# Kernel optimization log

Measured on AMD Instinct MI355X. Metric: run time of the kernel, lower is better.

Reference implementation:

```python
import jax, jax.numpy as jnp
from jax import lax
import numpy as np

GROUPS = 4


def _grid_sample_border(img, gx, gy):
    # img: [Bg, Cg, H, W]; gx, gy: [Bg, H, W] normalized grid in [-1, 1]
    # Replicates F.grid_sample(mode='bilinear', align_corners=False, padding_mode='border')
    Bg, Cg, H, W = img.shape
    ix = jnp.clip(((gx + 1.0) * W - 1.0) * 0.5, 0.0, W - 1.0)
    iy = jnp.clip(((gy + 1.0) * H - 1.0) * 0.5, 0.0, H - 1.0)
    x0 = jnp.floor(ix)
    y0 = jnp.floor(iy)
    wx = ix - x0
    wy = iy - y0
    x0i = x0.astype(jnp.int32)
    y0i = y0.astype(jnp.int32)
    x1i = jnp.minimum(x0i + 1, W - 1)
    y1i = jnp.minimum(y0i + 1, H - 1)

    def one(im, x0i, x1i, y0i, y1i, wx, wy):
        v00 = im[:, y0i, x0i]
        v01 = im[:, y0i, x1i]
        v10 = im[:, y1i, x0i]
        v11 = im[:, y1i, x1i]
        return (v00 * (1 - wx) * (1 - wy) + v01 * wx * (1 - wy)
                + v10 * (1 - wx) * wy + v11 * wx * wy)

    return jax.vmap(one)(img, x0i, x1i, y0i, y1i, wx, wy)


def setup_inputs() -> dict:
    key = jax.random.key(0)
    ks = jax.random.split(key, 8)
    B, N, C = 8, 4096, 768
    x = jax.random.normal(ks[0], (B, N, C), dtype=jnp.float32)
    dw_w = jax.random.normal(ks[1], (C, 1, 3, 3), dtype=jnp.float32) * 0.1  # depthwise kernel
    dw_b = jax.random.normal(ks[2], (C,), dtype=jnp.float32) * 0.1
    off_w = jax.random.normal(ks[3], (2 * GROUPS, C), dtype=jnp.float32) * 0.001  # std=0.001 init
    off_b = jnp.zeros((2 * GROUPS,), dtype=jnp.float32)
    wt_w = jax.random.normal(ks[4], (2 * GROUPS, C), dtype=jnp.float32) * 0.02
    wt_b = jnp.zeros((2 * GROUPS,), dtype=jnp.float32)
    offset_list = jnp.zeros((1,), dtype=jnp.int32)
    return {"x": x, "dw_w": dw_w, "dw_b": dw_b, "off_w": off_w, "off_b": off_b,
            "wt_w": wt_w, "wt_b": wt_b, "offset_list": offset_list,
            "patch_h": 64, "patch_w": 64}


def reference(x, dw_w, dw_b, off_w, off_b, wt_w, wt_b, offset_list, patch_h, patch_w):
    B, N, C = x.shape
    H, W = int(patch_h), int(patch_w)
    xi = jnp.transpose(x, (0, 2, 1)).reshape(B, C, H, W)

    # offset head: depthwise 3x3 conv -> GELU -> 1x1 conv to 2*groups channels
    dw = lax.conv_general_dilated(xi, dw_w, (1, 1), ((1, 1), (1, 1)),
                                  dimension_numbers=("NCHW", "OIHW", "NCHW"),
                                  feature_group_count=C)
    dw = jax.nn.gelu(dw + dw_b[None, :, None, None], approximate=False)
    off = jnp.einsum("bchw,oc->bohw", dw, off_w) + off_b[None, :, None, None]

    # weight head: 1x1 conv -> sigmoid
    wt = jax.nn.sigmoid(jnp.einsum("bchw,oc->bohw", xi, wt_w) + wt_b[None, :, None, None])

    off = (off * wt).reshape(B, 2, GROUPS, H, W)
    # fixed cross-shaped shifts: x-comp [0,0,-1,+1], y-comp [-1,+1,0,0]
    shifts = jnp.array([[0.0, 0.0, -1.0, 1.0], [-1.0, 1.0, 0.0, 0.0]],
                       dtype=x.dtype).reshape(1, 2, GROUPS, 1, 1)
    off = off + shifts

    cx = (jnp.arange(W, dtype=x.dtype) + 0.5)[None, None, None, :]  # pixel-center x coords
    cy = (jnp.arange(H, dtype=x.dtype) + 0.5)[None, None, :, None]  # pixel-center y coords
    gx = 2.0 * (cx + off[:, 0]) / W - 1.0  # [B, GROUPS, H, W]
    gy = 2.0 * (cy + off[:, 1]) / H - 1.0

    img = xi.reshape(B * GROUPS, C // GROUPS, H, W)
    samp = _grid_sample_border(img, gx.reshape(B * GROUPS, H, W),
                               gy.reshape(B * GROUPS, H, W))
    out = samp.reshape(B, C, N)
    return jnp.transpose(out, (0, 2, 1))  # [B, N, C]
```

## Files before the change

### kernel.cpp

```cpp
#include <hip/hip_runtime.h>
#include <math.h>

#define BB 8
#define CC 768
#define HH 64
#define WW 64
#define NN 4096
#define GG 4
#define NCHUNK 6
#define CHUNK 128

typedef __attribute__((ext_vector_type(8))) _Float16 half8;
typedef __attribute__((ext_vector_type(4))) float f32x4;

__device__ __forceinline__ float gelu_fast(float v) {
    const float z2 = 2.3022223f * v * fmaf(0.044715f, v * v, 1.0f);
    const float e = __builtin_amdgcn_exp2f(-z2);
    return __fdividef(v, 1.0f + e);
}

__global__ __launch_bounds__(128, 4) void dq_conv_mfma(
    const float* __restrict__ x,
    const float* __restrict__ dw_w,
    const float* __restrict__ dw_b,
    const float* __restrict__ off_w,
    const float* __restrict__ wt_w,
    float* __restrict__ offpart)
{
    __shared__ __attribute__((aligned(16))) _Float16 gl[2][16][144];
    __shared__ __attribute__((aligned(16))) _Float16 xh[2][16][144];
    const int t = threadIdx.x;
    const int lane = t & 63, wv = t >> 6;
    const int xcd = blockIdx.x & 7;
    const int local = blockIdx.x >> 3;
    const int chunk = local % NCHUNK;
    const int r = xcd * (BB * HH / 8) + local / NCHUNK;
    const int h = r & (HH - 1);
    const int b = r >> 6;
    const int c = chunk * CHUNK + t;

    const int n = lane & 15, kg = lane >> 4;
    const float* wsrc = (wv == 0) ? off_w : wt_w;
    half8 bfrag[4];
#pragma unroll
    for (int kt = 0; kt < 4; ++kt) {
        const bool valid = (n < 8);
        const float* src = wsrc + (valid ? n : 0) * CC + chunk * CHUNK + kt * 32 + kg * 8;
        half8 bf;
#pragma unroll
        for (int j = 0; j < 8; ++j) {
            bf[j] = (_Float16)(valid ? src[j] : 0.f);
        }
        bfrag[kt] = bf;
    }

    float w9[9];
#pragma unroll
    for (int j = 0; j < 9; ++j) w9[j] = dw_w[c * 9 + j];
    const float bias = dw_b[c];
    const bool tv = (h > 0), bv = (h < HH - 1);
    const float wt0 = tv ? w9[0] : 0.f, wt1 = tv ? w9[1] : 0.f, wt2 = tv ? w9[2] : 0.f;
    const float wb0 = bv ? w9[6] : 0.f, wb1 = bv ? w9[7] : 0.f, wb2 = bv ? w9[8] : 0.f;

    const float* base = x + (size_t)b * NN * CC + c;
    const float* rT = base + (size_t)((tv ? h - 1 : 0) * WW) * CC;
    const float* rM = base + (size_t)(h * WW) * CC;
    const float* rB = base + (size_t)((bv ? h + 1 : h) * WW) * CC;

    float cT[8], cM[8], cB[8], nT[8], nM[8], nB[8];
    float pT = 0.f, pM = 0.f, pB = 0.f;

#pragma unroll
    for (int j = 0; j < 8; ++j) {
        const size_t o = (size_t)j * CC;
        cT[j] = rT[o]; cM[j] = rM[o]; cB[j] = rB[o];
    }

#pragma unroll
    for (int q = 0; q < 4; ++q) {
        const int qb = q & 1;
#pragma unroll
        for (int hb = 0; hb < 2; ++hb) {
            const int wb = q * 2 + hb;
            if (wb < 7) {
#pragma unroll
                for (int j = 0; j < 8; ++j) {
                    const size_t o = (size_t)(wb * 8 + 8 + j) * CC;
                    nT[j] = rT[o]; nM[j] = rM[o]; nB[j] = rB[o];
                }
            } else {
#pragma unroll
                for (int j = 0; j < 8; ++j) { nT[j] = 0.f; nM[j] = 0.f; nB[j] = 0.f; }
            }
#pragma unroll
            for (int j = 0; j < 8; ++j) {
                const float lT = j ? cT[j - 1] : pT;
                const float lM = j ? cM[j - 1] : pM;
                const float lB = j ? cB[j - 1] : pB;
                const float rTv = (j == 7) ? nT[0] : cT[j + 1];
                const float rMv = (j == 7) ? nM[0] : cM[j + 1];
                const float rBv = (j == 7) ? nB[0] : cB[j + 1];
                const float conv = lT * wt0 + cT[j] * wt1 + rTv * wt2
                                 + lM * w9[3] + cM[j] * w9[4] + rMv * w9[5]
                                 + lB * wb0 + cB[j] * wb1 + rBv * wb2;
                const int colq = hb * 8 + j;
                gl[qb][colq][t] = (_Float16)gelu_fast(conv + bias);
                xh[qb][colq][t] = (_Float16)cM[j];
            }
            pT = cT[7]; pM = cM[7]; pB = cB[7];
#pragma unroll
            for (int j = 0; j < 8; ++j) { cT[j] = nT[j]; cM[j] = nM[j]; cB[j] = nB[j]; }
        }

        __syncthreads();
        f32x4 acc = {0.f, 0.f, 0.f, 0.f};
        if (wv == 0) {
#pragma unroll
            for (int kt = 0; kt < 4; ++kt) {
                const half8 a = *(const half8*)&gl[qb][n][kt * 32 + kg * 8];
                acc = __builtin_amdgcn_mfma_f32_16x16x32_f16(a, bfrag[kt], acc, 0, 0, 0);
            }
        } else {
#pragma unroll
            for (int kt = 0; kt < 4; ++kt) {
                const half8 a = *(const half8*)&xh[qb][n][kt * 32 + kg * 8];
                acc = __builtin_amdgcn_mfma_f32_16x16x32_f16(a, bfrag[kt], acc, 0, 0, 0);
            }
        }
        if (n < 8) {
            const int plane = chunk * 16 + (wv ? 8 + n : n);
            const size_t gpos = (size_t)(b * NN) + h * WW + q * 16 + kg * 4;
            float4 st; st.x = acc[0]; st.y = acc[1]; st.z = acc[2]; st.w = acc[3];
            *(float4*)&offpart[(size_t)plane * (BB * NN) + gpos] = st;
        }
    }
}

__global__ __launch_bounds__(256) void dq_combine(
    const float* __restrict__ offpart,
    const float* __restrict__ off_b,
    const float* __restrict__ wt_b,
    float* __restrict__ ixiy)
{
    const int t = threadIdx.x;
    const int o = t >> 5;
    const int gpos = blockIdx.x * 32 + (t & 31);
    const int b = gpos >> 12;
    const int hw = gpos & 4095;
    const int h = hw >> 6, w = hw & 63;

    float so = 0.f, sw = 0.f;
#pragma unroll
    for (int ch = 0; ch < NCHUNK; ++ch) {
        so += offpart[((size_t)(ch * 16 + o)) * (BB * NN) + gpos];
        sw += offpart[((size_t)(ch * 16 + 8 + o)) * (BB * NN) + gpos];
    }
    const float sig = 1.f / (1.f + __expf(-(sw + wt_b[o])));
    const float val = (so + off_b[o]) * sig;

    if (o < 4) {
        const float shx = (o == 2) ? -1.f : ((o == 3) ? 1.f : 0.f);
        const float ix = fminf(fmaxf((float)w + val + shx, 0.f), (float)(WW - 1));
        ixiy[(b * GG + o) * NN + hw] = ix;
    } else {
        const int g = o - 4;
        const float shy = (g == 0) ? -1.f : ((g == 1) ? 1.f : 0.f);
        const float iy = fminf(fmaxf((float)h + val + shy, 0.f), (float)(HH - 1));
        ixiy[BB * GG * NN + (b * GG + g) * NN + hw] = iy;
    }
}

__global__ __launch_bounds__(192) void dq_sample_vec(
    const float* __restrict__ x,
    const float* __restrict__ ixiy,
    float* __restrict__ out)
{
    __shared__ float ixy[8];
    const int t = threadIdx.x;
    const int p = (blockIdx.x & 7) * (BB * NN / 8) + (blockIdx.x >> 3);
    const int b = p >> 12;
    const int hw = p & 4095;

    if (t < 8) {
        const int g = t & 3;
        const int plane = (t >> 2) * (BB * GG * NN);
        ixy[t] = ixiy[plane + (b * GG + g) * NN + hw];
    }
    __syncthreads();

    const int g = t / 48;
    const float ix = ixy[g], iy = ixy[4 + g];
    const float x0f = floorf(ix), y0f = floorf(iy);
    const float wx = ix - x0f, wy = iy - y0f;
    const int x0 = (int)x0f, y0 = (int)y0f;
    const int x1 = min(x0 + 1, WW - 1), y1 = min(y0 + 1, HH - 1);
    const int c4 = t * 4;
    const float* xb = x + (size_t)b * NN * CC;
    const float4 v00 = *(const float4*)(xb + (size_t)(y0 * WW + x0) * CC + c4);
    const float4 v01 = *(const float4*)(xb + (size_t)(y0 * WW + x1) * CC + c4);
    const float4 v10 = *(const float4*)(xb + (size_t)(y1 * WW + x0) * CC + c4);
    const float4 v11 = *(const float4*)(xb + (size_t)(y1 * WW + x1) * CC + c4);
    const float w00 = (1.f - wx) * (1.f - wy), w01 = wx * (1.f - wy);
    const float w10 = (1.f - wx) * wy,         w11 = wx * wy;
    float4 r;
    r.x = v00.x * w00 + v01.x * w01 + v10.x * w10 + v11.x * w11;
    r.y = v00.y * w00 + v01.y * w01 + v10.y * w10 + v11.y * w11;
    r.z = v00.z * w00 + v01.z * w01 + v10.z * w10 + v11.z * w11;
    r.w = v00.w * w00 + v01.w * w01 + v10.w * w10 + v11.w * w11;
    *(float4*)(out + (size_t)p * CC + c4) = r;
}

__global__ __launch_bounds__(256) void dqshift_offsets_kernel(
    const float* __restrict__ x, const float* __restrict__ dw_w,
    const float* __restrict__ dw_b, const float* __restrict__ off_w,
    const float* __restrict__ off_b, const float* __restrict__ wt_w,
    const float* __restrict__ wt_b, float* __restrict__ ixiy)
{
    const int wave = threadIdx.x >> 6;
    const int lane = threadIdx.x & 63;
    const int p = blockIdx.x * 4 + wave;
    const int b = p >> 12;
    const int hw = p & 4095;
    const int h = hw >> 6;
    const int w = hw & 63;
    const float* xb = x + (size_t)b * NN * CC;
    float accO[8], accW[8];
#pragma unroll
    for (int o = 0; o < 8; ++o) { accO[o] = 0.f; accW[o] = 0.f; }
    for (int k = 0; k < CC / 64; ++k) {
        const int c = lane + (k << 6);
        float conv = 0.f, xc = 0.f;
#pragma unroll
        for (int dy = -1; dy <= 1; ++dy) {
            const int hh = h + dy;
            const bool vy = (hh >= 0) && (hh < HH);
#pragma unroll
            for (int dx = -1; dx <= 1; ++dx) {
                const int ww = w + dx;
                const bool vv = vy && (ww >= 0) && (ww < WW);
                const float tt = vv ? xb[(size_t)(hh * WW + ww) * CC + c] : 0.f;
                if (dy == 0 && dx == 0) xc = tt;
                conv = fmaf(tt, dw_w[c * 9 + (dy + 1) * 3 + (dx + 1)], conv);
            }
        }
        const float gv = conv + dw_b[c];
        const float gle = 0.5f * gv * (1.0f + erff(gv * 0.70710678118654752f));
#pragma unroll
        for (int o = 0; o < 8; ++o) {
            accO[o] = fmaf(gle, off_w[o * CC + c], accO[o]);
            accW[o] = fmaf(xc, wt_w[o * CC + c], accW[o]);
        }
    }
#pragma unroll
    for (int o = 0; o < 8; ++o) {
#pragma unroll
        for (int s = 32; s > 0; s >>= 1) {
            accO[o] += __shfl_xor(accO[o], s, 64);
            accW[o] += __shfl_xor(accW[o], s, 64);
        }
    }
    if (lane == 0) {
        const float shx[4] = {0.f, 0.f, -1.f, 1.f};
        const float shy[4] = {-1.f, 1.f, 0.f, 0.f};
#pragma unroll
        for (int g = 0; g < 4; ++g) {
            const float sx = 1.f / (1.f + expf(-(accW[g] + wt_b[g])));
            const float sy = 1.f / (1.f + expf(-(accW[4 + g] + wt_b[4 + g])));
            const float ox = (accO[g] + off_b[g]) * sx + shx[g];
            const float oy = (accO[4 + g] + off_b[4 + g]) * sy + shy[g];
            const float ix = fminf(fmaxf((float)w + ox, 0.f), (float)(WW - 1));
            const float iy = fminf(fmaxf((float)h + oy, 0.f), (float)(HH - 1));
            const int idx = (b * GG + g) * NN + hw;
            ixiy[idx] = ix;
            ixiy[BB * GG * NN + idx] = iy;
        }
    }
}

__global__ __launch_bounds__(256) void dqshift_sample_kernel(
    const float* __restrict__ x,
    const float* __restrict__ ixiy,
    float* __restrict__ out)
{
    const int p = blockIdx.x;
    const int b = p >> 12;
    const int hw = p & 4095;
    const float* xb = x + (size_t)b * NN * CC;
    float* ob = out + (size_t)p * CC;

#pragma unroll
    for (int k = 0; k < 3; ++k) {
        const int c = threadIdx.x + (k << 8);
        const int g = c / (CC / GG);
        const int idx = (b * GG + g) * NN + hw;
        const float ix = ixiy[idx];
        const float iy = ixiy[BB * GG * NN + idx];
        const float x0f = floorf(ix);
        const float y0f = floorf(iy);
        const float wx = ix - x0f;
        const float wy = iy - y0f;
        const int x0 = (int)x0f;
        const int y0 = (int)y0f;
        const int x1 = min(x0 + 1, WW - 1);
        const int y1 = min(y0 + 1, HH - 1);
        const float* r0 = xb + (size_t)(y0 * WW) * CC + c;
        const float* r1 = xb + (size_t)(y1 * WW) * CC + c;
        const float v00 = r0[(size_t)x0 * CC];
        const float v01 = r0[(size_t)x1 * CC];
        const float v10 = r1[(size_t)x0 * CC];
        const float v11 = r1[(size_t)x1 * CC];
        ob[c] = v00 * (1.f - wx) * (1.f - wy) + v01 * wx * (1.f - wy)
              + v10 * (1.f - wx) * wy + v11 * wx * wy;
    }
}

extern "C" void kernel_launch(void* const* d_in, const int* in_sizes, int n_in,
                              void* d_out, int out_size, void* d_ws, size_t ws_size,
                              hipStream_t stream) {
    const float* x     = (const float*)d_in[0];
    const float* dw_w  = (const float*)d_in[1];
    const float* dw_b  = (const float*)d_in[2];
    const float* off_w = (const float*)d_in[3];
    const float* off_b = (const float*)d_in[4];
    const float* wt_w  = (const float*)d_in[5];
    const float* wt_b  = (const float*)d_in[6];

    float* ixiy = (float*)d_ws;
    float* offpart = (float*)d_ws + 2 * BB * GG * NN;
    const size_t need = (size_t)(2 * BB * GG * NN + NCHUNK * 16 * BB * NN) * 4;

    if (ws_size >= need) {
        dq_conv_mfma<<<BB * HH * NCHUNK, 128, 0, stream>>>(
            x, dw_w, dw_b, off_w, wt_w, offpart);
        dq_combine<<<BB * NN / 32, 256, 0, stream>>>(
            offpart, off_b, wt_b, ixiy);
        dq_sample_vec<<<BB * NN, 192, 0, stream>>>(
            x, ixiy, (float*)d_out);
    } else {
        dqshift_offsets_kernel<<<BB * NN / 4, 256, 0, stream>>>(
            x, dw_w, dw_b, off_w, off_b, wt_w, wt_b, ixiy);
        dqshift_sample_kernel<<<BB * NN, 256, 0, stream>>>(x, ixiy, (float*)d_out);
    }
}
```

Baseline: 78.36 us.

## Materialize fp16 conv/GELU activations and run full-K MFMA GEMM per position

```diff
diff --git a/kernel.cpp b/kernel.cpp
--- a/kernel.cpp
+++ b/kernel.cpp
@@ -7,8 +7,8 @@
 #define WW 64
 #define NN 4096
 #define GG 4
-#define NCHUNK 6
-#define CHUNK 128
+#define KK 1536
+#define TPAD 1552
 
 typedef __attribute__((ext_vector_type(8))) _Float16 half8;
 typedef __attribute__((ext_vector_type(4))) float f32x4;
@@ -19,40 +19,29 @@
     return __fdividef(v, 1.0f + e);
 }
 
-__global__ __launch_bounds__(128, 4) void dq_conv_mfma(
+__global__ __launch_bounds__(256) void dq_wcvt(
+    const float* __restrict__ off_w, const float* __restrict__ wt_w,
+    _Float16* __restrict__ w16)
+{
+    const int i = blockIdx.x * 256 + threadIdx.x;
+    if (i < 8 * CC) w16[i] = (_Float16)off_w[i];
+    else            w16[i] = (_Float16)(wt_w[i - 8 * CC]);
+}
+
+__global__ __launch_bounds__(256) void dq_conv(
     const float* __restrict__ x,
     const float* __restrict__ dw_w,
     const float* __restrict__ dw_b,
-    const float* __restrict__ off_w,
-    const float* __restrict__ wt_w,
-    float* __restrict__ offpart)
-{
-    __shared__ __attribute__((aligned(16))) _Float16 gl[2][16][144];
-    __shared__ __attribute__((aligned(16))) _Float16 xh[2][16][144];
+    _Float16* __restrict__ g2)
+{
     const int t = threadIdx.x;
-    const int lane = t & 63, wv = t >> 6;
     const int xcd = blockIdx.x & 7;
     const int local = blockIdx.x >> 3;
-    const int chunk = local % NCHUNK;
-    const int r = xcd * (BB * HH / 8) + local / NCHUNK;
+    const int strip = local % 3;
+    const int r = xcd * (BB * HH / 8) + local / 3;
     const int h = r & (HH - 1);
     const int b = r >> 6;
-    const int c = chunk * CHUNK + t;
-
-    const int n = lane & 15, kg = lane >> 4;
-    const float* wsrc = (wv == 0) ? off_w : wt_w;
-    half8 bfrag[4];
-#pragma unroll
-    for (int kt = 0; kt < 4; ++kt) {
-        const bool valid = (n < 8);
-        const float* src = wsrc + (valid ? n : 0) * CC + chunk * CHUNK + kt * 32 + kg * 8;
-        half8 bf;
-#pragma unroll
-        for (int j = 0; j < 8; ++j) {
-            bf[j] = (_Float16)(valid ? src[j] : 0.f);
-        }
-        bfrag[kt] = bf;
-    }
+    const int c = strip * 256 + t;
 
     float w9[9];
 #pragma unroll
@@ -67,6 +56,8 @@
     const float* rM = base + (size_t)(h * WW) * CC;
     const float* rB = base + (size_t)((bv ? h + 1 : h) * WW) * CC;
 
+    _Float16* grow = g2 + (size_t)(b * NN + h * WW) * KK + c;
+
     float cT[8], cM[8], cB[8], nT[8], nM[8], nB[8];
     float pT = 0.f, pM = 0.f, pB = 0.f;
 
@@ -77,96 +68,100 @@
     }
 
 #pragma unroll
-    for (int q = 0; q < 4; ++q) {
-        const int qb = q & 1;
-#pragma unroll
-        for (int hb = 0; hb < 2; ++hb) {
-            const int wb = q * 2 + hb;
-            if (wb < 7) {
-#pragma unroll
-                for (int j = 0; j < 8; ++j) {
-                    const size_t o = (size_t)(wb * 8 + 8 + j) * CC;
-                    nT[j] = rT[o]; nM[j] = rM[o]; nB[j] = rB[o];
-                }
-            } else {
-#pragma unroll
-                for (int j = 0; j < 8; ++j) { nT[j] = 0.f; nM[j] = 0.f; nB[j] = 0.f; }
-            }
+    for (int wb = 0; wb < 8; ++wb) {
+        if (wb < 7) {
 #pragma unroll
             for (int j = 0; j < 8; ++j) {
-                const float lT = j ? cT[j - 1] : pT;
-                const float lM = j ? cM[j - 1] : pM;
-                const float lB = j ? cB[j - 1] : pB;
-                const float rTv = (j == 7) ? nT[0] : cT[j + 1];
-                const float rMv = (j == 7) ? nM[0] : cM[j + 1];
-                const float rBv = (j == 7) ? nB[0] : cB[j + 1];
-                const float conv = lT * wt0 + cT[j] * wt1 + rTv * wt2
-                                 + lM * w9[3] + cM[j] * w9[4] + rMv * w9[5]
-                                 + lB * wb0 + cB[j] * wb1 + rBv * wb2;
-                const int colq = hb * 8 + j;
-                gl[qb][colq][t] = (_Float16)gelu_fast(conv + bias);
-                xh[qb][colq][t] = (_Float16)cM[j];
-            }
-            pT = cT[7]; pM = cM[7]; pB = cB[7];
-#pragma unroll
-            for (int j = 0; j < 8; ++j) { cT[j] = nT[j]; cM[j] = nM[j]; cB[j] = nB[j]; }
-        }
-
-        __syncthreads();
-        f32x4 acc = {0.f, 0.f, 0.f, 0.f};
-        if (wv == 0) {
-#pragma unroll
-            for (int kt = 0; kt < 4; ++kt) {
-                const half8 a = *(const half8*)&gl[qb][n][kt * 32 + kg * 8];
-                acc = __builtin_amdgcn_mfma_f32_16x16x32_f16(a, bfrag[kt], acc, 0, 0, 0);
+                const size_t o = (size_t)(wb * 8 + 8 + j) * CC;
+                nT[j] = rT[o]; nM[j] = rM[o]; nB[j] = rB[o];
             }
         } else {
 #pragma unroll
-            for (int kt = 0; kt < 4; ++kt) {
-                const half8 a = *(const half8*)&xh[qb][n][kt * 32 + kg * 8];
-                acc = __builtin_amdgcn_mfma_f32_16x16x32_f16(a, bfrag[kt], acc, 0, 0, 0);
-            }
-        }
-        if (n < 8) {
-            const int plane = chunk * 16 + (wv ? 8 + n : n);
-            const size_t gpos = (size_t)(b * NN) + h * WW + q * 16 + kg * 4;
-            float4 st; st.x = acc[0]; st.y = acc[1]; st.z = acc[2]; st.w = acc[3];
-            *(float4*)&offpart[(size_t)plane * (BB * NN) + gpos] = st;
-        }
-    }
-}
-
-__global__ __launch_bounds__(256) void dq_combine(
-    const float* __restrict__ offpart,
+            for (int j = 0; j < 8; ++j) { nT[j] = 0.f; nM[j] = 0.f; nB[j] = 0.f; }
+        }
+#pragma unroll
+        for (int j = 0; j < 8; ++j) {
+            const float lT = j ? cT[j - 1] : pT;
+            const float lM = j ? cM[j - 1] : pM;
+            const float lB = j ? cB[j - 1] : pB;
+            const float rTv = (j == 7) ? nT[0] : cT[j + 1];
+            const float rMv = (j == 7) ? nM[0] : cM[j + 1];
+            const float rBv = (j == 7) ? nB[0] : cB[j + 1];
+            const float conv = lT * wt0 + cT[j] * wt1 + rTv * wt2
+                             + lM * w9[3] + cM[j] * w9[4] + rMv * w9[5]
+                             + lB * wb0 + cB[j] * wb1 + rBv * wb2;
+            const size_t po = (size_t)(wb * 8 + j) * KK;
+            grow[po]       = (_Float16)gelu_fast(conv + bias);
+            grow[po + CC]  = (_Float16)cM[j];
+        }
+        pT = cT[7]; pM = cM[7]; pB = cB[7];
+#pragma unroll
+        for (int j = 0; j < 8; ++j) { cT[j] = nT[j]; cM[j] = nM[j]; cB[j] = nB[j]; }
+    }
+}
+
+__global__ __launch_bounds__(128) void dq_gemm(
+    const _Float16* __restrict__ g2,
+    const _Float16* __restrict__ w16,
     const float* __restrict__ off_b,
     const float* __restrict__ wt_b,
     float* __restrict__ ixiy)
 {
+    __shared__ __attribute__((aligned(16))) _Float16 tile[16][TPAD];
+    __shared__ float exw[16][8];
     const int t = threadIdx.x;
-    const int o = t >> 5;
-    const int gpos = blockIdx.x * 32 + (t & 31);
-    const int b = gpos >> 12;
-    const int hw = gpos & 4095;
-    const int h = hw >> 6, w = hw & 63;
-
-    float so = 0.f, sw = 0.f;
-#pragma unroll
-    for (int ch = 0; ch < NCHUNK; ++ch) {
-        so += offpart[((size_t)(ch * 16 + o)) * (BB * NN) + gpos];
-        sw += offpart[((size_t)(ch * 16 + 8 + o)) * (BB * NN) + gpos];
-    }
-    const float sig = 1.f / (1.f + __expf(-(sw + wt_b[o])));
-    const float val = (so + off_b[o]) * sig;
-
-    if (o < 4) {
-        const float shx = (o == 2) ? -1.f : ((o == 3) ? 1.f : 0.f);
-        const float ix = fminf(fmaxf((float)w + val + shx, 0.f), (float)(WW - 1));
-        ixiy[(b * GG + o) * NN + hw] = ix;
-    } else {
-        const int g = o - 4;
-        const float shy = (g == 0) ? -1.f : ((g == 1) ? 1.f : 0.f);
-        const float iy = fminf(fmaxf((float)h + val + shy, 0.f), (float)(HH - 1));
-        ixiy[BB * GG * NN + (b * GG + g) * NN + hw] = iy;
+    const int lane = t & 63, wv = t >> 6;
+    const int p0 = blockIdx.x * 16;
+    const int b = p0 >> 12;
+    const int hw0 = p0 & 4095;
+    const int h = hw0 >> 6, w0 = hw0 & 63;
+
+    const half8* src = (const half8*)(g2 + (size_t)p0 * KK);
+#pragma unroll
+    for (int it = 0; it < 24; ++it) {
+        const int ci = it * 128 + t;
+        const int row = ci / 192, col = ci % 192;
+        *(half8*)&tile[row][col * 8] = src[(size_t)row * 192 + col];
+    }
+    __syncthreads();
+
+    const int n = lane & 15, kg = lane >> 4;
+    const bool valid = (n < 8);
+    const int koff = wv * CC;
+    const _Float16* wrow = w16 + (size_t)wv * 8 * CC + (valid ? n : 0) * CC;
+
+    f32x4 acc = {0.f, 0.f, 0.f, 0.f};
+#pragma unroll
+    for (int kt = 0; kt < 24; ++kt) {
+        const half8 a = *(const half8*)&tile[n][koff + kt * 32 + kg * 8];
+        const half8 bf = *(const half8*)&wrow[kt * 32 + kg * 8];
+        acc = __builtin_amdgcn_mfma_f32_16x16x32_f16(a, bf, acc, 0, 0, 0);
+    }
+
+    if (wv == 1 && valid) {
+#pragma unroll
+        for (int j = 0; j < 4; ++j) exw[kg * 4 + j][n] = acc[j];
+    }
+    __syncthreads();
+    if (wv == 0 && valid) {
+        const float ob = off_b[n], wbv = wt_b[n];
+#pragma unroll
+        for (int j = 0; j < 4; ++j) {
+            const int pos = kg * 4 + j;
+            const float wt = exw[pos][n];
+            const float sig = __fdividef(1.f, 1.f + __builtin_amdgcn_exp2f(-1.4426950f * (wt + wbv)));
+            const float val = (acc[j] + ob) * sig;
+            const int w = w0 + pos;
+            const int hwp = h * WW + w;
+            if (n < 4) {
+                const float shx = (n == 2) ? -1.f : ((n == 3) ? 1.f : 0.f);
+                ixiy[(b * GG + n) * NN + hwp] = fminf(fmaxf((float)w + val + shx, 0.f), (float)(WW - 1));
+            } else {
+                const int g = n - 4;
+                const float shy = (g == 0) ? -1.f : ((g == 1) ? 1.f : 0.f);
+                ixiy[BB * GG * NN + (b * GG + g) * NN + hwp] = fminf(fmaxf((float)h + val + shy, 0.f), (float)(HH - 1));
+            }
+        }
     }
 }
 
@@ -202,12 +197,12 @@
     const float4 v11 = *(const float4*)(xb + (size_t)(y1 * WW + x1) * CC + c4);
     const float w00 = (1.f - wx) * (1.f - wy), w01 = wx * (1.f - wy);
     const float w10 = (1.f - wx) * wy,         w11 = wx * wy;
-    float4 r;
-    r.x = v00.x * w00 + v01.x * w01 + v10.x * w10 + v11.x * w11;
-    r.y = v00.y * w00 + v01.y * w01 + v10.y * w10 + v11.y * w11;
-    r.z = v00.z * w00 + v01.z * w01 + v10.z * w10 + v11.z * w11;
-    r.w = v00.w * w00 + v01.w * w01 + v10.w * w10 + v11.w * w11;
-    *(float4*)(out + (size_t)p * CC + c4) = r;
+    float4 rr;
+    rr.x = v00.x * w00 + v01.x * w01 + v10.x * w10 + v11.x * w11;
+    rr.y = v00.y * w00 + v01.y * w01 + v10.y * w10 + v11.y * w11;
+    rr.z = v00.z * w00 + v01.z * w01 + v10.z * w10 + v11.z * w11;
+    rr.w = v00.w * w00 + v01.w * w01 + v10.w * w10 + v11.w * w11;
+    *(float4*)(out + (size_t)p * CC + c4) = rr;
 }
 
 __global__ __launch_bounds__(256) void dqshift_offsets_kernel(
@@ -326,16 +321,15 @@
     const float* wt_b  = (const float*)d_in[6];
 
     float* ixiy = (float*)d_ws;
-    float* offpart = (float*)d_ws + 2 * BB * GG * NN;
-    const size_t need = (size_t)(2 * BB * GG * NN + NCHUNK * 16 * BB * NN) * 4;
+    _Float16* w16 = (_Float16*)((char*)d_ws + 1048576);
+    _Float16* g2  = (_Float16*)((char*)d_ws + 1048576 + 32768);
+    const size_t need = 1048576 + 32768 + (size_t)BB * NN * KK * 2;
 
     if (ws_size >= need) {
-        dq_conv_mfma<<<BB * HH * NCHUNK, 128, 0, stream>>>(
-            x, dw_w, dw_b, off_w, wt_w, offpart);
-        dq_combine<<<BB * NN / 32, 256, 0, stream>>>(
-            offpart, off_b, wt_b, ixiy);
-        dq_sample_vec<<<BB * NN, 192, 0, stream>>>(
-            x, ixiy, (float*)d_out);
+        dq_wcvt<<<48, 256, 0, stream>>>(off_w, wt_w, w16);
+        dq_conv<<<BB * HH * 3, 256, 0, stream>>>(x, dw_w, dw_b, g2);
+        dq_gemm<<<BB * NN / 16, 128, 0, stream>>>(g2, w16, off_b, wt_b, ixiy);
+        dq_sample_vec<<<BB * NN, 192, 0, stream>>>(x, ixiy, (float*)d_out);
     } else {
         dqshift_offsets_kernel<<<BB * NN / 4, 256, 0, stream>>>(
             x, dw_w, dw_b, off_w, off_b, wt_w, wt_b, ixiy);
```

Result: slower. 100.9 us (+28.7%).
